# Optimization experiments

Hardware: AMD Instinct MI355X
Metric: run time of the kernel (lower is better)

## Reference

```python
import jax, jax.numpy as jnp
import numpy as np

B, S, P, HID, HQ, HKV, D, MAXP = 8, 4, 4096, 4096, 32, 8, 128, 8192


def setup_inputs() -> dict:
    key = jax.random.key(0)
    ks = jax.random.split(key, 8)
    # rotary tables (Llama-style: freqs duplicated across halves)
    inv_freq = 1.0 / (10000.0 ** (jnp.arange(0, D // 2, dtype=jnp.float32) / (D // 2)))
    t = jnp.arange(MAXP, dtype=jnp.float32)
    emb = jnp.concatenate([jnp.outer(t, inv_freq)] * 2, axis=-1)  # [MAXP, D]
    w = 0.02
    return {
        "x": jax.random.normal(ks[0], (B, S, HID), dtype=jnp.float32),
        "wq": w * jax.random.normal(ks[1], (HID, HQ * D), dtype=jnp.float32),
        "wk": w * jax.random.normal(ks[2], (HID, HKV * D), dtype=jnp.float32),
        "wv": w * jax.random.normal(ks[3], (HID, HKV * D), dtype=jnp.float32),
        "wo": w * jax.random.normal(ks[4], (HQ * D, HID), dtype=jnp.float32),
        "cos": jnp.cos(emb),
        "sin": jnp.sin(emb),
        "k_cache": jax.random.normal(ks[5], (B, P, HKV, D), dtype=jnp.float32),
        "v_cache": jax.random.normal(ks[6], (B, P, HKV, D), dtype=jnp.float32),
        "past_len": P,
    }


def _rope(x, c, s):
    # x: [B,S,H,D]; c,s: [1,S,1,D] -- half-rotation RoPE
    half = x.shape[-1] // 2
    x1, x2 = x[..., :half], x[..., half:]
    return x * c + jnp.concatenate([-x2, x1], axis=-1) * s


def reference(x, wq, wk, wv, wo, cos, sin, k_cache, v_cache, past_len):
    b, s, _ = x.shape
    hq, hkv, d = HQ, HKV, D
    q = (x @ wq).reshape(b, s, hq, d)
    k = (x @ wk).reshape(b, s, hkv, d)
    v = (x @ wv).reshape(b, s, hkv, d)

    pos = past_len + jnp.arange(s)                     # new-token positions
    c = cos[pos][None, :, None, :]
    sn = sin[pos][None, :, None, :]
    q = _rope(q, c, sn)
    k = _rope(k, c, sn)

    # append new kv to cache
    k_all = jnp.concatenate([k_cache, k], axis=1)      # [B,T,HKV,D]
    v_all = jnp.concatenate([v_cache, v], axis=1)
    t_len = k_all.shape[1]

    group = hq // hkv
    qg = q.reshape(b, s, hkv, group, d)
    scores = jnp.einsum('bskgd,btkd->bkgst', qg, k_all) / jnp.sqrt(jnp.asarray(d, x.dtype))

    # causal: query at position past_len+i attends to key positions <= past_len+i
    key_pos = jnp.arange(t_len)
    mask = pos[:, None] >= key_pos[None, :]            # [S,T]
    scores = jnp.where(mask[None, None, None], scores, jnp.asarray(-1e30, scores.dtype))
    attn = jax.nn.softmax(scores, axis=-1)

    out = jnp.einsum('bkgst,btkd->bskgd', attn, v_all).reshape(b, s, hq * d)
    return out @ wo
```

## Files before the change

kernel.cpp:

```cpp
#include <hip/hip_runtime.h>
#include <math.h>

#define NB 8
#define NS 4
#define NP 4096
#define HID 4096
#define NHQ 32
#define NHKV 8
#define ND 128
#define NGROUP 4
#define NBS 32
#define NQI 16
#define NCHUNK 9
#define TCHUNK 512
#define LOG2E 1.4426950408889634f

__global__ __launch_bounds__(256) void prep_xT(const float* __restrict__ x,
                                               float* __restrict__ xT) {
  int n = blockIdx.x * 256 + threadIdx.x;
  int r = n >> 12;
  int k = n & 4095;
  xT[k * NBS + r] = x[n];
}

__global__ __launch_bounds__(256) void rope_kernel(
    const float* __restrict__ qb, const float* __restrict__ kb,
    const float* __restrict__ cosp, const float* __restrict__ sinp,
    const int* __restrict__ past_len, float* __restrict__ q_t,
    float* __restrict__ k_new) {
  int n = blockIdx.x * 256 + threadIdx.x;
  int pl = past_len[0];
  if (n < NBS * HID) {
    int r = n >> 12;
    int hd = n & 4095;
    int h = hd >> 7, d = hd & 127;
    int b = r >> 2, s = r & 3;
    int pos = pl + s;
    float c = cosp[pos * ND + d], sn = sinp[pos * ND + d];
    float v = qb[n];
    float other = (d < 64) ? -qb[n + 64] : qb[n - 64];
    float rv = fmaf(v, c, other * sn);
    int kv = h >> 2, g = h & 3;
    q_t[(((b * NHKV + kv) * ND + d) * NQI) + g * NS + s] = rv;
  } else {
    n -= NBS * HID;
    int r = n >> 10;
    int hd = n & 1023;
    int kv = hd >> 7, d = hd & 127;
    int b = r >> 2, s = r & 3;
    int pos = pl + s;
    float c = cosp[pos * ND + d], sn = sinp[pos * ND + d];
    float v = kb[n];
    float other = (d < 64) ? -kb[n + 64] : kb[n - 64];
    k_new[((b * NHKV + kv) * NS + s) * ND + d] = fmaf(v, c, other * sn);
  }
}

__global__ __launch_bounds__(256) void gemm32(
    const float* __restrict__ xT, const float* __restrict__ wq,
    const float* __restrict__ wk, const float* __restrict__ wv,
    const float* __restrict__ wo, float* __restrict__ qb,
    float* __restrict__ kb2, float* __restrict__ vb, float* __restrict__ outp,
    int mode) {
  __shared__ float accl[4][64][33];
  int cb = blockIdx.x, kblk = blockIdx.y;
  const float* __restrict__ W;
  float* ob;
  int ld, col0;
  if (mode) {
    W = wo; ld = 4096; ob = outp; col0 = cb * 64;
  } else if (cb < 64) {
    W = wq; ld = 4096; ob = qb; col0 = cb * 64;
  } else if (cb < 80) {
    W = wk; ld = 1024; ob = kb2; col0 = (cb - 64) * 64;
  } else {
    W = wv; ld = 1024; ob = vb; col0 = (cb - 80) * 64;
  }
  int tid = threadIdx.x;
  int lane = tid & 63;
  int wid = __builtin_amdgcn_readfirstlane(tid >> 6);
  int k0 = kblk * 512 + wid * 128;
  const float* wp = W + (size_t)k0 * ld + col0 + lane;
  const float* xp = xT + (size_t)k0 * NBS;
  float acc[NBS];
#pragma unroll
  for (int m = 0; m < NBS; m++) acc[m] = 0.f;
#pragma unroll 4
  for (int kk = 0; kk < 128; ++kk) {
    float w = wp[(size_t)kk * ld];
    const float* xr = xp + kk * NBS;
#pragma unroll
    for (int m = 0; m < NBS; m++) acc[m] = fmaf(xr[m], w, acc[m]);
  }
#pragma unroll
  for (int m = 0; m < NBS; m++) accl[wid][lane][m] = acc[m];
  __syncthreads();
#pragma unroll
  for (int j = 0; j < 8; j++) {
    int o = j * 256 + tid;
    int c = o & 63, m = o >> 6;
    float s = accl[0][c][m] + accl[1][c][m] + accl[2][c][m] + accl[3][c][m];
    atomicAdd(&ob[(size_t)m * ld + col0 + c], s);
  }
}

__global__ __launch_bounds__(256) void attn_kernel(
    const float* __restrict__ q_t, const float* __restrict__ k_cache,
    const float* __restrict__ v_cache, const float* __restrict__ k_new,
    const float* __restrict__ vb, float* __restrict__ part_o,
    float* __restrict__ part_m, float* __restrict__ part_l) {
  __shared__ float p_lds[TCHUNK * 17];
  __shared__ float redm[NQI][4];
  __shared__ float redl[NQI][4];
  int blk = blockIdx.x;
  int chunk = blk % NCHUNK;
  int bk = blk / NCHUNK;
  int b = bk >> 3, kv = bk & 7;
  int tid = threadIdx.x;
  int lane = tid & 63;
  int wid = __builtin_amdgcn_readfirstlane(tid >> 6);
  bool last = (chunk == 8);
  int tcount = last ? NS : TCHUNK;
  const float* qbase = q_t + (size_t)bk * ND * NQI;
  float sc[2][NQI];
#pragma unroll
  for (int r = 0; r < 2; r++) {
    int t_loc = r * 256 + tid;
    bool valid = t_loc < tcount;
    int t_eff = valid ? t_loc : 0;
    const float* kp =
        last ? (k_new + ((size_t)bk * NS + t_eff) * ND)
             : (k_cache +
                (((size_t)b * NP + chunk * TCHUNK + t_eff) * NHKV + kv) * ND);
    float s_acc[NQI];
#pragma unroll
    for (int i = 0; i < NQI; i++) s_acc[i] = 0.f;
    for (int d4 = 0; d4 < 32; ++d4) {
      float4 kvv = *(const float4*)(kp + d4 * 4);
      const float* qp = qbase + (d4 * 4) * NQI;
#pragma unroll
      for (int i = 0; i < NQI; i++) {
        float s = s_acc[i];
        s = fmaf(kvv.x, qp[i], s);
        s = fmaf(kvv.y, qp[NQI + i], s);
        s = fmaf(kvv.z, qp[2 * NQI + i], s);
        s = fmaf(kvv.w, qp[3 * NQI + i], s);
        s_acc[i] = s;
      }
    }
    const float scale = 0.08838834764831845f;
#pragma unroll
    for (int i = 0; i < NQI; i++) {
      float sv = s_acc[i] * scale;
      if (!valid || (last && t_loc > (i & 3))) sv = -__builtin_inff();
      sc[r][i] = sv;
    }
  }
#pragma unroll
  for (int i = 0; i < NQI; i++) {
    float m = fmaxf(sc[0][i], sc[1][i]);
#pragma unroll
    for (int off = 1; off < 64; off <<= 1) m = fmaxf(m, __shfl_xor(m, off, 64));
    if (lane == 0) redm[i][wid] = m;
  }
  __syncthreads();
  float l_loc[NQI];
#pragma unroll
  for (int i = 0; i < NQI; i++) {
    float m_i = fmaxf(fmaxf(redm[i][0], redm[i][1]),
                      fmaxf(redm[i][2], redm[i][3]));
    float p0 = exp2f((sc[0][i] - m_i) * LOG2E);
    float p1 = exp2f((sc[1][i] - m_i) * LOG2E);
    p_lds[(size_t)tid * 17 + i] = p0;
    p_lds[(size_t)(256 + tid) * 17 + i] = p1;
    l_loc[i] = p0 + p1;
  }
#pragma unroll
  for (int i = 0; i < NQI; i++) {
    float l = l_loc[i];
#pragma unroll
    for (int off = 1; off < 64; off <<= 1) l += __shfl_xor(l, off, 64);
    if (lane == 0) redl[i][wid] = l;
  }
  __syncthreads();
  int g8 = tid >> 5;
  int i0 = g8 * 2;
  int dq = (tid & 31) * 4;
  float o0[4] = {0, 0, 0, 0}, o1[4] = {0, 0, 0, 0};
  for (int t = 0; t < tcount; ++t) {
    const float* vp =
        last ? (vb + ((size_t)b * NS + t) * (NHKV * ND) + kv * ND)
             : (v_cache +
                (((size_t)b * NP + chunk * TCHUNK + t) * NHKV + kv) * ND);
    float4 vv = *(const float4*)(vp + dq);
    float p0 = p_lds[(size_t)t * 17 + i0];
    float p1 = p_lds[(size_t)t * 17 + i0 + 1];
    o0[0] = fmaf(p0, vv.x, o0[0]); o0[1] = fmaf(p0, vv.y, o0[1]);
    o0[2] = fmaf(p0, vv.z, o0[2]); o0[3] = fmaf(p0, vv.w, o0[3]);
    o1[0] = fmaf(p1, vv.x, o1[0]); o1[1] = fmaf(p1, vv.y, o1[1]);
    o1[2] = fmaf(p1, vv.z, o1[2]); o1[3] = fmaf(p1, vv.w, o1[3]);
  }
  size_t obase = (size_t)blk * (NQI * ND);
#pragma unroll
  for (int j = 0; j < 4; j++) {
    part_o[obase + (size_t)i0 * ND + dq + j] = o0[j];
    part_o[obase + (size_t)(i0 + 1) * ND + dq + j] = o1[j];
  }
  if (tid < NQI) {
    int i = tid;
    float m_i = fmaxf(fmaxf(redm[i][0], redm[i][1]),
                      fmaxf(redm[i][2], redm[i][3]));
    float l_i = redl[i][0] + redl[i][1] + redl[i][2] + redl[i][3];
    part_m[(size_t)blk * NQI + i] = m_i;
    part_l[(size_t)blk * NQI + i] = l_i;
  }
}

__global__ __launch_bounds__(256) void combine_kernel(
    const float* __restrict__ part_o, const float* __restrict__ part_m,
    const float* __restrict__ part_l, float* __restrict__ attn_T) {
  int bk = blockIdx.x;
  int tid = threadIdx.x;
  int i = tid >> 4;
  int d8 = (tid & 15) * 8;
  float M = -__builtin_inff();
#pragma unroll
  for (int c = 0; c < NCHUNK; c++)
    M = fmaxf(M, part_m[((size_t)bk * NCHUNK + c) * NQI + i]);
  float L = 0.f;
  float o[8] = {0, 0, 0, 0, 0, 0, 0, 0};
#pragma unroll
  for (int c = 0; c < NCHUNK; c++) {
    size_t pc = (size_t)bk * NCHUNK + c;
    float mc = part_m[pc * NQI + i];
    float w = exp2f((mc - M) * LOG2E);
    L = fmaf(part_l[pc * NQI + i], w, L);
    const float* po = part_o + pc * (NQI * ND) + (size_t)i * ND + d8;
#pragma unroll
    for (int j = 0; j < 8; j++) o[j] = fmaf(w, po[j], o[j]);
  }
  float inv = 1.0f / L;
  int b = bk >> 3, kv = bk & 7;
  int g = i >> 2, s = i & 3;
  int h = kv * NGROUP + g;
  int r = b * NS + s;
#pragma unroll
  for (int j = 0; j < 8; j++)
    attn_T[(size_t)(h * ND + d8 + j) * NBS + r] = o[j] * inv;
}

extern "C" void kernel_launch(void* const* d_in, const int* in_sizes, int n_in,
                              void* d_out, int out_size, void* d_ws,
                              size_t ws_size, hipStream_t stream) {
  const float* x = (const float*)d_in[0];
  const float* wq = (const float*)d_in[1];
  const float* wk = (const float*)d_in[2];
  const float* wv = (const float*)d_in[3];
  const float* wo = (const float*)d_in[4];
  const float* cosp = (const float*)d_in[5];
  const float* sinp = (const float*)d_in[6];
  const float* k_cache = (const float*)d_in[7];
  const float* v_cache = (const float*)d_in[8];
  const int* past_len = (const int*)d_in[9];
  float* out = (float*)d_out;

  float* ws = (float*)d_ws;
  float* xT = ws;
  float* qb = xT + 131072;
  float* kb = qb + 131072;
  float* vb = kb + 32768;
  float* q_t = vb + 32768;
  float* k_new = q_t + 131072;
  float* attn_T = k_new + 32768;
  float* part_o = attn_T + 131072;
  float* part_m = part_o + 1179648;
  float* part_l = part_m + 9216;

  hipMemsetAsync(qb, 0, (131072 + 32768 + 32768) * sizeof(float), stream);
  hipMemsetAsync(out, 0, (size_t)NBS * HID * sizeof(float), stream);

  prep_xT<<<512, 256, 0, stream>>>(x, xT);
  gemm32<<<dim3(96, 8), 256, 0, stream>>>(xT, wq, wk, wv, wo, qb, kb, vb, out,
                                          0);
  rope_kernel<<<640, 256, 0, stream>>>(qb, kb, cosp, sinp, past_len, q_t,
                                       k_new);
  attn_kernel<<<64 * NCHUNK, 256, 0, stream>>>(q_t, k_cache, v_cache, k_new,
                                               vb, part_o, part_m, part_l);
  combine_kernel<<<64, 256, 0, stream>>>(part_o, part_m, part_l, attn_T);
  gemm32<<<dim3(64, 8), 256, 0, stream>>>(attn_T, wq, wk, wv, wo, qb, kb, vb,
                                          out, 1);
}
```

Before: 503.7 us.

## Replace atomic split-K GEMM with partial buffers and reduce; finer attention chunks

The QKV and output projections now write split-K partial sums (16 K-splits, 128 columns per block, float2 weight loads) to a workspace, followed by separate reduce kernels. This removes the memsets and atomicAdds of the earlier version. Attention moves to 256-token chunks with 512-thread blocks in which two threads split each key's dot product, which gives more blocks and shorter per-thread PV loops. The combine step is also split across two blocks per head group. The cost is extra workspace traffic, two additional kernel launches, and more chunks for the combine kernel to merge.

```diff
diff --git a/kernel.cpp b/kernel.cpp
--- a/kernel.cpp
+++ b/kernel.cpp
@@ -11,8 +11,10 @@
 #define NGROUP 4
 #define NBS 32
 #define NQI 16
-#define NCHUNK 9
-#define TCHUNK 512
+#define NCHUNK 17
+#define TCHUNK 256
+#define KSPLIT 16
+#define QKV_COLS 6144
 #define LOG2E 1.4426950408889634f
 
 __global__ __launch_bounds__(256) void prep_xT(const float* __restrict__ x,
@@ -56,164 +58,211 @@
   }
 }
 
-__global__ __launch_bounds__(256) void gemm32(
-    const float* __restrict__ xT, const float* __restrict__ wq,
+__global__ __launch_bounds__(256) void gemm_part(
+    const float* __restrict__ A_T, const float* __restrict__ wq,
     const float* __restrict__ wk, const float* __restrict__ wv,
-    const float* __restrict__ wo, float* __restrict__ qb,
-    float* __restrict__ kb2, float* __restrict__ vb, float* __restrict__ outp,
-    int mode) {
-  __shared__ float accl[4][64][33];
-  int cb = blockIdx.x, kblk = blockIdx.y;
-  const float* __restrict__ W;
-  float* ob;
-  int ld, col0;
+    const float* __restrict__ wo, float* __restrict__ P, int mode) {
+  __shared__ float lds[2 * 64 * 64];
+  int cb = blockIdx.x, kb = blockIdx.y;
+  int ncols = mode ? 4096 : QKV_COLS;
+  int col0 = cb * 128;
+  const float* W;
+  int ld, wcol;
   if (mode) {
-    W = wo; ld = 4096; ob = outp; col0 = cb * 64;
-  } else if (cb < 64) {
-    W = wq; ld = 4096; ob = qb; col0 = cb * 64;
-  } else if (cb < 80) {
-    W = wk; ld = 1024; ob = kb2; col0 = (cb - 64) * 64;
+    W = wo; ld = 4096; wcol = col0;
+  } else if (col0 < 4096) {
+    W = wq; ld = 4096; wcol = col0;
+  } else if (col0 < 5120) {
+    W = wk; ld = 1024; wcol = col0 - 4096;
   } else {
-    W = wv; ld = 1024; ob = vb; col0 = (cb - 80) * 64;
+    W = wv; ld = 1024; wcol = col0 - 5120;
   }
   int tid = threadIdx.x;
   int lane = tid & 63;
   int wid = __builtin_amdgcn_readfirstlane(tid >> 6);
-  int k0 = kblk * 512 + wid * 128;
-  const float* wp = W + (size_t)k0 * ld + col0 + lane;
-  const float* xp = xT + (size_t)k0 * NBS;
-  float acc[NBS];
-#pragma unroll
-  for (int m = 0; m < NBS; m++) acc[m] = 0.f;
-#pragma unroll 4
-  for (int kk = 0; kk < 128; ++kk) {
-    float w = wp[(size_t)kk * ld];
+  int k0 = kb * 256 + wid * 64;
+  const float* wp = W + (size_t)k0 * ld + wcol + lane * 2;
+  const float* xp = A_T + (size_t)k0 * NBS;
+  float acc[64];
+#pragma unroll
+  for (int v = 0; v < 64; v++) acc[v] = 0.f;
+#pragma unroll 2
+  for (int kk = 0; kk < 64; ++kk) {
+    float2 w2 = *(const float2*)(wp + (size_t)kk * ld);
     const float* xr = xp + kk * NBS;
 #pragma unroll
-    for (int m = 0; m < NBS; m++) acc[m] = fmaf(xr[m], w, acc[m]);
-  }
-#pragma unroll
-  for (int m = 0; m < NBS; m++) accl[wid][lane][m] = acc[m];
-  __syncthreads();
-#pragma unroll
-  for (int j = 0; j < 8; j++) {
-    int o = j * 256 + tid;
-    int c = o & 63, m = o >> 6;
-    float s = accl[0][c][m] + accl[1][c][m] + accl[2][c][m] + accl[3][c][m];
-    atomicAdd(&ob[(size_t)m * ld + col0 + c], s);
-  }
-}
-
-__global__ __launch_bounds__(256) void attn_kernel(
+    for (int m = 0; m < NBS; m++) {
+      acc[2 * m] = fmaf(xr[m], w2.x, acc[2 * m]);
+      acc[2 * m + 1] = fmaf(xr[m], w2.y, acc[2 * m + 1]);
+    }
+  }
+  if (wid >= 2) {
+#pragma unroll
+    for (int v = 0; v < 64; v++) lds[(wid - 2) * 4096 + v * 64 + lane] = acc[v];
+  }
+  __syncthreads();
+  if (wid < 2) {
+#pragma unroll
+    for (int v = 0; v < 64; v++) acc[v] += lds[wid * 4096 + v * 64 + lane];
+  }
+  __syncthreads();
+  if (wid == 1) {
+#pragma unroll
+    for (int v = 0; v < 64; v++) lds[v * 64 + lane] = acc[v];
+  }
+  __syncthreads();
+  if (wid == 0) {
+#pragma unroll
+    for (int v = 0; v < 64; v++) acc[v] += lds[v * 64 + lane];
+#pragma unroll
+    for (int m = 0; m < NBS; m++) {
+      float2 st = make_float2(acc[2 * m], acc[2 * m + 1]);
+      *(float2*)(P + ((size_t)kb * NBS + m) * ncols + col0 + lane * 2) = st;
+    }
+  }
+}
+
+__global__ __launch_bounds__(256) void reduce_qkv(const float* __restrict__ P,
+                                                  float* __restrict__ qb,
+                                                  float* __restrict__ kbuf,
+                                                  float* __restrict__ vbuf) {
+  size_t idx = ((size_t)blockIdx.x * 256 + threadIdx.x) * 4;
+  float4 s = make_float4(0.f, 0.f, 0.f, 0.f);
+#pragma unroll
+  for (int p = 0; p < KSPLIT; p++) {
+    float4 v = *(const float4*)(P + (size_t)p * (NBS * QKV_COLS) + idx);
+    s.x += v.x; s.y += v.y; s.z += v.z; s.w += v.w;
+  }
+  int r = (int)(idx / QKV_COLS);
+  int col = (int)(idx % QKV_COLS);
+  float* dst;
+  if (col < 4096)
+    dst = qb + (size_t)r * 4096 + col;
+  else if (col < 5120)
+    dst = kbuf + (size_t)r * 1024 + (col - 4096);
+  else
+    dst = vbuf + (size_t)r * 1024 + (col - 5120);
+  *(float4*)dst = s;
+}
+
+__global__ __launch_bounds__(256) void reduce_o(const float* __restrict__ P,
+                                                float* __restrict__ outp) {
+  size_t idx = ((size_t)blockIdx.x * 256 + threadIdx.x) * 4;
+  float4 s = make_float4(0.f, 0.f, 0.f, 0.f);
+#pragma unroll
+  for (int p = 0; p < KSPLIT; p++) {
+    float4 v = *(const float4*)(P + (size_t)p * (NBS * 4096) + idx);
+    s.x += v.x; s.y += v.y; s.z += v.z; s.w += v.w;
+  }
+  *(float4*)(outp + idx) = s;
+}
+
+__global__ __launch_bounds__(512, 6) void attn_kernel(
     const float* __restrict__ q_t, const float* __restrict__ k_cache,
     const float* __restrict__ v_cache, const float* __restrict__ k_new,
-    const float* __restrict__ vb, float* __restrict__ part_o,
+    const float* __restrict__ vbuf, float* __restrict__ part_o,
     float* __restrict__ part_m, float* __restrict__ part_l) {
   __shared__ float p_lds[TCHUNK * 17];
-  __shared__ float redm[NQI][4];
-  __shared__ float redl[NQI][4];
+  __shared__ float redm[NQI][8];
+  __shared__ float redl[NQI][8];
+  __shared__ float mfin[NQI];
   int blk = blockIdx.x;
   int chunk = blk % NCHUNK;
   int bk = blk / NCHUNK;
   int b = bk >> 3, kv = bk & 7;
   int tid = threadIdx.x;
   int lane = tid & 63;
-  int wid = __builtin_amdgcn_readfirstlane(tid >> 6);
-  bool last = (chunk == 8);
+  int wid = tid >> 6;
+  bool last = (chunk == NCHUNK - 1);
   int tcount = last ? NS : TCHUNK;
-  const float* qbase = q_t + (size_t)bk * ND * NQI;
-  float sc[2][NQI];
-#pragma unroll
-  for (int r = 0; r < 2; r++) {
-    int t_loc = r * 256 + tid;
-    bool valid = t_loc < tcount;
-    int t_eff = valid ? t_loc : 0;
-    const float* kp =
-        last ? (k_new + ((size_t)bk * NS + t_eff) * ND)
-             : (k_cache +
-                (((size_t)b * NP + chunk * TCHUNK + t_eff) * NHKV + kv) * ND);
-    float s_acc[NQI];
-#pragma unroll
-    for (int i = 0; i < NQI; i++) s_acc[i] = 0.f;
-    for (int d4 = 0; d4 < 32; ++d4) {
-      float4 kvv = *(const float4*)(kp + d4 * 4);
-      const float* qp = qbase + (d4 * 4) * NQI;
-#pragma unroll
-      for (int i = 0; i < NQI; i++) {
-        float s = s_acc[i];
-        s = fmaf(kvv.x, qp[i], s);
-        s = fmaf(kvv.y, qp[NQI + i], s);
-        s = fmaf(kvv.z, qp[2 * NQI + i], s);
-        s = fmaf(kvv.w, qp[3 * NQI + i], s);
-        s_acc[i] = s;
-      }
+  const float* qbase = q_t + (size_t)bk * (ND * NQI);
+
+  int t_loc = tid >> 1;
+  int half = tid & 1;
+  bool valid = t_loc < tcount;
+  int t_eff = valid ? t_loc : 0;
+  const float* kp =
+      last ? (k_new + ((size_t)bk * NS + t_eff) * ND + half * 64)
+           : (k_cache +
+              (((size_t)b * NP + chunk * TCHUNK + t_eff) * NHKV + kv) * ND +
+              half * 64);
+  float s_acc[NQI];
+#pragma unroll
+  for (int i = 0; i < NQI; i++) s_acc[i] = 0.f;
+#pragma unroll 4
+  for (int d4 = 0; d4 < 16; ++d4) {
+    float4 kvv = *(const float4*)(kp + d4 * 4);
+    const float* qp = qbase + (half * 64 + d4 * 4) * NQI;
+#pragma unroll
+    for (int i = 0; i < NQI; i++) {
+      float s = s_acc[i];
+      s = fmaf(kvv.x, qp[i], s);
+      s = fmaf(kvv.y, qp[NQI + i], s);
+      s = fmaf(kvv.z, qp[2 * NQI + i], s);
+      s = fmaf(kvv.w, qp[3 * NQI + i], s);
+      s_acc[i] = s;
     }
-    const float scale = 0.08838834764831845f;
-#pragma unroll
-    for (int i = 0; i < NQI; i++) {
-      float sv = s_acc[i] * scale;
-      if (!valid || (last && t_loc > (i & 3))) sv = -__builtin_inff();
-      sc[r][i] = sv;
-    }
-  }
+  }
+  const float scale = 0.08838834764831845f;
+  float sc[NQI];
 #pragma unroll
   for (int i = 0; i < NQI; i++) {
-    float m = fmaxf(sc[0][i], sc[1][i]);
+    float s = s_acc[i] + __shfl_xor(s_acc[i], 1, 64);
+    s *= scale;
+    if (!valid || (last && t_loc > (i & 3))) s = -__builtin_inff();
+    sc[i] = s;
+  }
+#pragma unroll
+  for (int i = 0; i < NQI; i++) {
+    float m = sc[i];
 #pragma unroll
     for (int off = 1; off < 64; off <<= 1) m = fmaxf(m, __shfl_xor(m, off, 64));
     if (lane == 0) redm[i][wid] = m;
   }
   __syncthreads();
-  float l_loc[NQI];
+  if (tid < NQI) {
+    float m = redm[tid][0];
+#pragma unroll
+    for (int w = 1; w < 8; w++) m = fmaxf(m, redm[tid][w]);
+    mfin[tid] = m;
+  }
+  __syncthreads();
 #pragma unroll
   for (int i = 0; i < NQI; i++) {
-    float m_i = fmaxf(fmaxf(redm[i][0], redm[i][1]),
-                      fmaxf(redm[i][2], redm[i][3]));
-    float p0 = exp2f((sc[0][i] - m_i) * LOG2E);
-    float p1 = exp2f((sc[1][i] - m_i) * LOG2E);
-    p_lds[(size_t)tid * 17 + i] = p0;
-    p_lds[(size_t)(256 + tid) * 17 + i] = p1;
-    l_loc[i] = p0 + p1;
-  }
-#pragma unroll
-  for (int i = 0; i < NQI; i++) {
-    float l = l_loc[i];
-#pragma unroll
-    for (int off = 1; off < 64; off <<= 1) l += __shfl_xor(l, off, 64);
-    if (lane == 0) redl[i][wid] = l;
-  }
-  __syncthreads();
-  int g8 = tid >> 5;
-  int i0 = g8 * 2;
+    float p = exp2f((sc[i] - mfin[i]) * LOG2E);
+    if (half == 0) p_lds[t_loc * 17 + i] = p;
+    float lp = (half == 0) ? p : 0.f;
+#pragma unroll
+    for (int off = 1; off < 64; off <<= 1) lp += __shfl_xor(lp, off, 64);
+    if (lane == 0) redl[i][wid] = lp;
+  }
+  __syncthreads();
+  if (tid < NQI) {
+    float l = redl[tid][0];
+#pragma unroll
+    for (int w = 1; w < 8; w++) l += redl[tid][w];
+    part_m[(size_t)blk * NQI + tid] = mfin[tid];
+    part_l[(size_t)blk * NQI + tid] = l;
+  }
+
+  int i0 = tid >> 5;
   int dq = (tid & 31) * 4;
-  float o0[4] = {0, 0, 0, 0}, o1[4] = {0, 0, 0, 0};
+  const float* vpb =
+      last ? (vbuf + (size_t)b * NS * (NHKV * ND) + kv * ND + dq)
+           : (v_cache + ((size_t)b * NP + chunk * TCHUNK) * (NHKV * ND) +
+              kv * ND + dq);
+  float o0 = 0.f, o1 = 0.f, o2 = 0.f, o3 = 0.f;
+#pragma unroll 4
   for (int t = 0; t < tcount; ++t) {
-    const float* vp =
-        last ? (vb + ((size_t)b * NS + t) * (NHKV * ND) + kv * ND)
-             : (v_cache +
-                (((size_t)b * NP + chunk * TCHUNK + t) * NHKV + kv) * ND);
-    float4 vv = *(const float4*)(vp + dq);
-    float p0 = p_lds[(size_t)t * 17 + i0];
-    float p1 = p_lds[(size_t)t * 17 + i0 + 1];
-    o0[0] = fmaf(p0, vv.x, o0[0]); o0[1] = fmaf(p0, vv.y, o0[1]);
-    o0[2] = fmaf(p0, vv.z, o0[2]); o0[3] = fmaf(p0, vv.w, o0[3]);
-    o1[0] = fmaf(p1, vv.x, o1[0]); o1[1] = fmaf(p1, vv.y, o1[1]);
-    o1[2] = fmaf(p1, vv.z, o1[2]); o1[3] = fmaf(p1, vv.w, o1[3]);
-  }
-  size_t obase = (size_t)blk * (NQI * ND);
-#pragma unroll
-  for (int j = 0; j < 4; j++) {
-    part_o[obase + (size_t)i0 * ND + dq + j] = o0[j];
-    part_o[obase + (size_t)(i0 + 1) * ND + dq + j] = o1[j];
-  }
-  if (tid < NQI) {
-    int i = tid;
-    float m_i = fmaxf(fmaxf(redm[i][0], redm[i][1]),
-                      fmaxf(redm[i][2], redm[i][3]));
-    float l_i = redl[i][0] + redl[i][1] + redl[i][2] + redl[i][3];
-    part_m[(size_t)blk * NQI + i] = m_i;
-    part_l[(size_t)blk * NQI + i] = l_i;
-  }
+    float4 vv = *(const float4*)(vpb + (size_t)t * (NHKV * ND));
+    float p = p_lds[t * 17 + i0];
+    o0 = fmaf(p, vv.x, o0);
+    o1 = fmaf(p, vv.y, o1);
+    o2 = fmaf(p, vv.z, o2);
+    o3 = fmaf(p, vv.w, o3);
+  }
+  float4 st = make_float4(o0, o1, o2, o3);
+  *(float4*)(part_o + (size_t)blk * (NQI * ND) + (size_t)i0 * ND + dq) = st;
 }
 
 __global__ __launch_bounds__(256) void combine_kernel(
@@ -222,31 +271,34 @@
   int bk = blockIdx.x;
   int tid = threadIdx.x;
   int i = tid >> 4;
-  int d8 = (tid & 15) * 8;
+  int dh = (tid & 15) * 4 + blockIdx.y * 64;
   float M = -__builtin_inff();
 #pragma unroll
   for (int c = 0; c < NCHUNK; c++)
     M = fmaxf(M, part_m[((size_t)bk * NCHUNK + c) * NQI + i]);
   float L = 0.f;
-  float o[8] = {0, 0, 0, 0, 0, 0, 0, 0};
+  float o0 = 0.f, o1 = 0.f, o2 = 0.f, o3 = 0.f;
 #pragma unroll
   for (int c = 0; c < NCHUNK; c++) {
     size_t pc = (size_t)bk * NCHUNK + c;
     float mc = part_m[pc * NQI + i];
     float w = exp2f((mc - M) * LOG2E);
     L = fmaf(part_l[pc * NQI + i], w, L);
-    const float* po = part_o + pc * (NQI * ND) + (size_t)i * ND + d8;
-#pragma unroll
-    for (int j = 0; j < 8; j++) o[j] = fmaf(w, po[j], o[j]);
+    float4 po = *(const float4*)(part_o + pc * (NQI * ND) + (size_t)i * ND + dh);
+    o0 = fmaf(w, po.x, o0);
+    o1 = fmaf(w, po.y, o1);
+    o2 = fmaf(w, po.z, o2);
+    o3 = fmaf(w, po.w, o3);
   }
   float inv = 1.0f / L;
   int b = bk >> 3, kv = bk & 7;
   int g = i >> 2, s = i & 3;
   int h = kv * NGROUP + g;
   int r = b * NS + s;
-#pragma unroll
-  for (int j = 0; j < 8; j++)
-    attn_T[(size_t)(h * ND + d8 + j) * NBS + r] = o[j] * inv;
+  attn_T[(size_t)(h * ND + dh + 0) * NBS + r] = o0 * inv;
+  attn_T[(size_t)(h * ND + dh + 1) * NBS + r] = o1 * inv;
+  attn_T[(size_t)(h * ND + dh + 2) * NBS + r] = o2 * inv;
+  attn_T[(size_t)(h * ND + dh + 3) * NBS + r] = o3 * inv;
 }
 
 extern "C" void kernel_launch(void* const* d_in, const int* in_sizes, int n_in,
@@ -267,26 +319,28 @@
   float* ws = (float*)d_ws;
   float* xT = ws;
   float* qb = xT + 131072;
-  float* kb = qb + 131072;
-  float* vb = kb + 32768;
-  float* q_t = vb + 32768;
+  float* kbuf = qb + 131072;
+  float* vbuf = kbuf + 32768;
+  float* q_t = vbuf + 32768;
   float* k_new = q_t + 131072;
   float* attn_T = k_new + 32768;
-  float* part_o = attn_T + 131072;
-  float* part_m = part_o + 1179648;
-  float* part_l = part_m + 9216;
-
-  hipMemsetAsync(qb, 0, (131072 + 32768 + 32768) * sizeof(float), stream);
-  hipMemsetAsync(out, 0, (size_t)NBS * HID * sizeof(float), stream);
+  float* R = attn_T + 131072;
+  float* Pq = R;
+  float* part_o = R;
+  float* part_m = R + 2228224;
+  float* part_l = part_m + 17408;
+  float* Po = R;
 
   prep_xT<<<512, 256, 0, stream>>>(x, xT);
-  gemm32<<<dim3(96, 8), 256, 0, stream>>>(xT, wq, wk, wv, wo, qb, kb, vb, out,
-                                          0);
-  rope_kernel<<<640, 256, 0, stream>>>(qb, kb, cosp, sinp, past_len, q_t,
+  gemm_part<<<dim3(48, KSPLIT), 256, 0, stream>>>(xT, wq, wk, wv, wo, Pq, 0);
+  reduce_qkv<<<192, 256, 0, stream>>>(Pq, qb, kbuf, vbuf);
+  rope_kernel<<<640, 256, 0, stream>>>(qb, kbuf, cosp, sinp, past_len, q_t,
                                        k_new);
-  attn_kernel<<<64 * NCHUNK, 256, 0, stream>>>(q_t, k_cache, v_cache, k_new,
-                                               vb, part_o, part_m, part_l);
-  combine_kernel<<<64, 256, 0, stream>>>(part_o, part_m, part_l, attn_T);
-  gemm32<<<dim3(64, 8), 256, 0, stream>>>(attn_T, wq, wk, wv, wo, qb, kb, vb,
-                                          out, 1);
-}
+  attn_kernel<<<64 * NCHUNK, 512, 0, stream>>>(q_t, k_cache, v_cache, k_new,
+                                               vbuf, part_o, part_m, part_l);
+  combine_kernel<<<dim3(64, 2), 256, 0, stream>>>(part_o, part_m, part_l,
+                                                  attn_T);
+  gemm_part<<<dim3(32, KSPLIT), 256, 0, stream>>>(attn_T, wq, wk, wv, wo, Po,
+                                                  1);
+  reduce_o<<<128, 256, 0, stream>>>(Po, out);
+}
```

Measured after the change: 640.1 us. +27.1%, slower.
